# Kernel optimization log

Measured on AMD Instinct MI355X. Metric: run time of the kernel, lower is better.

The kernel has to match this reference:

```python
import jax, jax.numpy as jnp
import numpy as np

EMBED_DIM = 1024
NUM_HEADS = 16
HEAD_DIM = EMBED_DIM // NUM_HEADS


def setup_inputs() -> dict:
    key = jax.random.key(0)
    ks = jax.random.split(key, 9)
    B, S, E, hd = 2, 2048, EMBED_DIM, HEAD_DIM
    s_e = 1.0 / np.sqrt(E)
    return {
        "x": jax.random.normal(ks[0], (B, S, E), dtype=jnp.float32),
        "wq": jax.random.uniform(ks[1], (E, E), jnp.float32, -s_e, s_e),
        "bq": jax.random.uniform(ks[2], (E,), jnp.float32, -s_e, s_e),
        "wk": jax.random.uniform(ks[3], (E, hd), jnp.float32, -s_e, s_e),
        "bk": jax.random.uniform(ks[4], (hd,), jnp.float32, -s_e, s_e),
        "wv": jax.random.uniform(ks[5], (E, hd), jnp.float32, -s_e, s_e),
        "bv": jax.random.uniform(ks[6], (hd,), jnp.float32, -s_e, s_e),
        "wo": jax.random.uniform(ks[7], (E, E), jnp.float32, -s_e, s_e),
        "bo": jax.random.uniform(ks[8], (E,), jnp.float32, -s_e, s_e),
    }


def reference(x, wq, bq, wk, bk, wv, bv, wo, bo):
    B, S, E = x.shape
    H, hd = NUM_HEADS, HEAD_DIM
    # projections
    q = (x @ wq + bq).reshape(B, S, H, hd)          # [B,S,H,hd]
    k = x @ wk + bk                                  # [B,S,hd] shared across heads
    v = x @ wv + bv                                  # [B,S,hd]
    scale = 1.0 / np.sqrt(hd).astype(np.float32)
    # scores: [B,H,S_q,S_k]
    scores = jnp.einsum('bqhd,bkd->bhqk', q, k) * scale
    attn = jax.nn.softmax(scores, axis=-1)
    out = jnp.einsum('bhqk,bkd->bqhd', attn, v).reshape(B, S, E)
    return out @ wo + bo
```

## Files before the change

### kernel.cpp

```cpp
#include <hip/hip_runtime.h>
#include <stdint.h>

#define SLEN 2048
#define EDIM 1024
#define NH 16
#define HD 64
#define QLD 1152

typedef unsigned short u16;
typedef short bf8 __attribute__((ext_vector_type(8)));
typedef float f4 __attribute__((ext_vector_type(4)));
typedef bf8 bf8_a __attribute__((may_alias));
typedef uint2 uint2_a __attribute__((may_alias));
typedef uint4 uint4_a __attribute__((may_alias));

__device__ __forceinline__ u16 f2bf(float x) {
  union { __bf16 h; u16 u; } c; c.h = (__bf16)x; return c.u;
}
__device__ __forceinline__ unsigned pk2bf(float a, float b) {
  union { __bf16 h[2]; unsigned u; } c;
  c.h[0] = (__bf16)a; c.h[1] = (__bf16)b;
  return c.u;
}
__device__ __forceinline__ void async_cp16(u16* lds, const u16* g) {
  __builtin_amdgcn_global_load_lds((__attribute__((address_space(1))) void*)g,
                                   (__attribute__((address_space(3))) void*)lds,
                                   16, 0, 0);
}

__global__ void convert_x(const float* __restrict__ src, u16* __restrict__ dst) {
  const int i = (blockIdx.x * 256 + threadIdx.x) * 8;
  u16 tmp[8];
#pragma unroll
  for (int j = 0; j < 8; ++j) tmp[j] = f2bf(src[i + j]);
  *(uint4_a*)&dst[i] = *(const uint4_a*)tmp;
}

__device__ __forceinline__ void tcvt_tile(const float* src, int srcLd,
                                          u16* dst, int dstLd, int r0, int c0) {
  __shared__ u16 tile[64][65];
  const int t = threadIdx.x;
#pragma unroll
  for (int i = 0; i < 16; ++i) {
    int e = i * 256 + t, rr = e >> 6, cc = e & 63;
    tile[rr][cc] = f2bf(src[(size_t)(r0 + rr) * srcLd + c0 + cc]);
  }
  __syncthreads();
#pragma unroll
  for (int i = 0; i < 16; ++i) {
    int e = i * 256 + t, j = e >> 6, ii = e & 63;
    dst[(size_t)(c0 + j) * dstLd + r0 + ii] = tile[ii][j];
  }
}

__global__ void prep_w(const float* wq, const float* wk, const float* wv,
                       const float* wo, const float* bq, const float* bk,
                       const float* bv, const float* bo,
                       u16* wT, u16* woT, float* bQKV, float* bOut) {
  const int yy = blockIdx.y;
  if (yy < 16) tcvt_tile(wq, 1024, wT, 1024, blockIdx.x * 64, yy * 64);
  else if (yy < 32) tcvt_tile(wo, 1024, woT, 1024, blockIdx.x * 64, (yy - 16) * 64);
  else if (yy == 32) tcvt_tile(wk, 64, wT + (size_t)1024 * 1024, 1024, blockIdx.x * 64, 0);
  else if (yy == 33) tcvt_tile(wv, 64, wT + (size_t)1088 * 1024, 1024, blockIdx.x * 64, 0);
  else {
    int i = blockIdx.x * 256 + threadIdx.x;
    if (i < 1024) bQKV[i] = bq[i];
    else if (i < 1088) bQKV[i] = bk[i - 1024];
    else if (i < 1152) bQKV[i] = bv[i - 1088];
    int j = i - 1152;
    if (j >= 0 && j < 1024) bOut[j] = bo[j];
  }
}

__global__ __launch_bounds__(256) void gemm_bt_bias(
    const u16* __restrict__ A, const u16* __restrict__ Bt,
    const float* __restrict__ bias, void* __restrict__ C, int K, int ldc,
    int ofp32, u16* __restrict__ vtb) {
  __shared__ __align__(16) u16 As[64 * 64];
  __shared__ __align__(16) u16 Bs[128 * 64];
  const int tn0 = blockIdx.x * 128, tm0 = blockIdx.y * 64;
  const int tid = threadIdx.x, wave = tid >> 6, lane = tid & 63;
  const int quad = lane >> 4, l16 = lane & 15;
  const int wm = wave & 1, wn = wave >> 1;

  f4 acc[2][4];
#pragma unroll
  for (int i = 0; i < 2; ++i)
#pragma unroll
    for (int j = 0; j < 4; ++j) acc[i][j] = f4{0.f, 0.f, 0.f, 0.f};

  int aslot[2], bslot[4]; size_t aoff[2], boff[4];
#pragma unroll
  for (int i = 0; i < 2; ++i) {
    int s = i * 256 + tid, m = s >> 3, kc = s & 7, c = (kc - m) & 7;
    aslot[i] = s; aoff[i] = (size_t)(tm0 + m) * K + c * 8;
  }
#pragma unroll
  for (int i = 0; i < 4; ++i) {
    int s = i * 256 + tid, n = s >> 3, kc = s & 7, c = (kc - n) & 7;
    bslot[i] = s; boff[i] = (size_t)(tn0 + n) * K + c * 8;
  }
  int ard[2][2], brd[4][2];
#pragma unroll
  for (int mi = 0; mi < 2; ++mi) {
    int m = wm * 32 + mi * 16 + l16;
#pragma unroll
    for (int kk = 0; kk < 2; ++kk)
      ard[mi][kk] = (m * 8 + (((kk * 4 + quad) + m) & 7)) * 8;
  }
#pragma unroll
  for (int ni = 0; ni < 4; ++ni) {
    int n = wn * 64 + ni * 16 + l16;
#pragma unroll
    for (int kk = 0; kk < 2; ++kk)
      brd[ni][kk] = (n * 8 + (((kk * 4 + quad) + n) & 7)) * 8;
  }

  const int kIt = K >> 6;
  for (int it = 0; it < kIt; ++it) {
    __syncthreads();
    const size_t kb = (size_t)it * 64;
#pragma unroll
    for (int i = 0; i < 2; ++i) async_cp16(&As[aslot[i] * 8], A + aoff[i] + kb);
#pragma unroll
    for (int i = 0; i < 4; ++i) async_cp16(&Bs[bslot[i] * 8], Bt + boff[i] + kb);
    __syncthreads();
#pragma unroll
    for (int kk = 0; kk < 2; ++kk) {
      bf8 af[2], bfr[4];
#pragma unroll
      for (int mi = 0; mi < 2; ++mi) af[mi] = *(const bf8_a*)&As[ard[mi][kk]];
#pragma unroll
      for (int ni = 0; ni < 4; ++ni) bfr[ni] = *(const bf8_a*)&Bs[brd[ni][kk]];
#pragma unroll
      for (int mi = 0; mi < 2; ++mi)
#pragma unroll
        for (int ni = 0; ni < 4; ++ni)
          acc[mi][ni] = __builtin_amdgcn_mfma_f32_16x16x32_bf16(
              af[mi], bfr[ni], acc[mi][ni], 0, 0, 0);
    }
  }

  float bv[4];
#pragma unroll
  for (int ni = 0; ni < 4; ++ni) bv[ni] = bias[tn0 + wn * 64 + ni * 16 + l16];
#pragma unroll
  for (int mi = 0; mi < 2; ++mi) {
    int row0 = tm0 + wm * 32 + mi * 16 + quad * 4;
#pragma unroll
    for (int ni = 0; ni < 4; ++ni) {
      int col = tn0 + wn * 64 + ni * 16 + l16;
      float vv[4];
#pragma unroll
      for (int r = 0; r < 4; ++r) vv[r] = acc[mi][ni][r] + bv[ni];
      if (ofp32) {
#pragma unroll
        for (int r = 0; r < 4; ++r)
          ((float*)C)[(size_t)(row0 + r) * ldc + col] = vv[r];
      } else {
#pragma unroll
        for (int r = 0; r < 4; ++r)
          ((u16*)C)[(size_t)(row0 + r) * ldc + col] = f2bf(vv[r]);
      }
      if (vtb != nullptr && col >= 1088) {
        int d = col - 1088, bb = row0 >> 11, s0 = row0 & 2047;
        uint2 pk;
        pk.x = pk2bf(vv[0], vv[1]);
        pk.y = pk2bf(vv[2], vv[3]);
        *(uint2_a*)&vtb[(size_t)(bb * 64 + d) * SLEN + s0] = pk;
      }
    }
  }
}

__global__ __launch_bounds__(256, 4) void attn_kernel(
    const u16* __restrict__ qkv, const u16* __restrict__ vT,
    u16* __restrict__ aout) {
  __shared__ __align__(16) u16 Kf[8192];
  __shared__ __align__(16) u16 Vf[8192];
  __shared__ __align__(16) u16 Ps[4096];
  const int qt = blockIdx.x, bh = blockIdx.y, b = bh >> 4, h = bh & 15;
  const int tid = threadIdx.x, wave = tid >> 6, lane = tid & 63;
  const int quad = lane >> 4, l16 = lane & 15;

#pragma unroll
  for (int i = 0; i < 4; ++i) {
    int d = i * 256 + tid;
    int kk = d >> 9, g = (d >> 6) & 7, qd = (d >> 4) & 3, r16 = d & 15;
    async_cp16(&Kf[d * 8],
               qkv + (size_t)(b * SLEN + qt * 128 + g * 16 + r16) * QLD +
                   h * HD + (kk * 4 + qd) * 8);
  }
  __syncthreads();
  bf8 bq[2][2];
#pragma unroll
  for (int nt = 0; nt < 2; ++nt)
#pragma unroll
    for (int kk = 0; kk < 2; ++kk)
      bq[nt][kk] = *(const bf8_a*)&Kf[((kk * 8 + wave * 2 + nt) * 64 + lane) * 8];

  f4 acc_o[2][4];
#pragma unroll
  for (int i = 0; i < 2; ++i)
#pragma unroll
    for (int j = 0; j < 4; ++j) acc_o[i][j] = f4{0.f, 0.f, 0.f, 0.f};
  f4 lr4[2] = {f4{0.f, 0.f, 0.f, 0.f}, f4{0.f, 0.f, 0.f, 0.f}};
  const float C1 = 0.125f * 1.44269504089f;
  const int psb = wave * 1024;

  for (int kt = 0; kt < 16; ++kt) {
    __syncthreads();
#pragma unroll
    for (int i = 0; i < 4; ++i) {
      int d = i * 256 + tid;
      int kk = d >> 9, k8 = (d >> 6) & 7, qd = (d >> 4) & 3, r16 = d & 15;
      async_cp16(&Kf[d * 8],
                 qkv + (size_t)(b * SLEN + kt * 128 + k8 * 16 + r16) * QLD +
                     EDIM + (kk * 4 + qd) * 8);
    }
#pragma unroll
    for (int i = 0; i < 4; ++i) {
      int d = i * 256 + tid;
      int k4 = d >> 8, ni = (d >> 6) & 3, qd = (d >> 4) & 3, r16 = d & 15;
      async_cp16(&Vf[d * 8],
                 vT + (size_t)(b * 64 + ni * 16 + r16) * SLEN + kt * 128 +
                     (k4 * 4 + qd) * 8);
    }
    __syncthreads();

#pragma unroll
    for (int k4 = 0; k4 < 4; ++k4) {
      f4 st[2][2];
#pragma unroll
      for (int j = 0; j < 2; ++j)
#pragma unroll
        for (int nt = 0; nt < 2; ++nt) st[j][nt] = f4{0.f, 0.f, 0.f, 0.f};
#pragma unroll
      for (int kk = 0; kk < 2; ++kk)
#pragma unroll
        for (int j = 0; j < 2; ++j) {
          bf8 ak = *(const bf8_a*)&Kf[((kk * 8 + k4 * 2 + j) * 64 + lane) * 8];
#pragma unroll
          for (int nt = 0; nt < 2; ++nt)
            st[j][nt] = __builtin_amdgcn_mfma_f32_16x16x32_bf16(
                ak, bq[nt][kk], st[j][nt], 0, 0, 0);
        }
#pragma unroll
      for (int nt = 0; nt < 2; ++nt)
#pragma unroll
        for (int j = 0; j < 2; ++j) {
          f4 pe;
          pe[0] = __builtin_amdgcn_exp2f(st[j][nt][0] * C1);
          pe[1] = __builtin_amdgcn_exp2f(st[j][nt][1] * C1);
          pe[2] = __builtin_amdgcn_exp2f(st[j][nt][2] * C1);
          pe[3] = __builtin_amdgcn_exp2f(st[j][nt][3] * C1);
          lr4[nt] += pe;
          uint2 pk;
          pk.x = pk2bf(pe[0], pe[1]);
          pk.y = pk2bf(pe[2], pe[3]);
          int qd2 = j * 2 + (quad >> 1);
          *(uint2_a*)&Ps[psb + ((nt * 4 + qd2) * 16 + l16) * 8 + (quad & 1) * 4] = pk;
        }
      asm volatile("" ::: "memory");
      bf8 ap[2];
#pragma unroll
      for (int mt = 0; mt < 2; ++mt)
        ap[mt] = *(const bf8_a*)&Ps[psb + ((mt * 4 + quad) * 16 + l16) * 8];
#pragma unroll
      for (int ni = 0; ni < 4; ++ni) {
        bf8 bv = *(const bf8_a*)&Vf[((k4 * 4 + ni) * 64 + lane) * 8];
#pragma unroll
        for (int mt = 0; mt < 2; ++mt)
          acc_o[mt][ni] = __builtin_amdgcn_mfma_f32_16x16x32_bf16(
              ap[mt], bv, acc_o[mt][ni], 0, 0, 0);
      }
      asm volatile("" ::: "memory");
    }
  }

  float ls[2];
#pragma unroll
  for (int nt = 0; nt < 2; ++nt) {
    float s = (lr4[nt][0] + lr4[nt][1]) + (lr4[nt][2] + lr4[nt][3]);
    s += __shfl_xor(s, 16, 64);
    s += __shfl_xor(s, 32, 64);
    ls[nt] = s;
  }
#pragma unroll
  for (int mt = 0; mt < 2; ++mt)
#pragma unroll
    for (int r = 0; r < 4; ++r) {
      float li = __shfl(ls[mt], quad * 4 + r, 64);
      float inv = 1.f / li;
      size_t row = (size_t)(b * SLEN + qt * 128 + wave * 32 + mt * 16 + quad * 4 + r);
#pragma unroll
      for (int ni = 0; ni < 4; ++ni)
        aout[row * EDIM + h * HD + ni * 16 + l16] = f2bf(acc_o[mt][ni][r] * inv);
    }
}

extern "C" void kernel_launch(void* const* d_in, const int* in_sizes, int n_in,
                              void* d_out, int out_size, void* d_ws, size_t ws_size,
                              hipStream_t stream) {
  const float* x  = (const float*)d_in[0];
  const float* wq = (const float*)d_in[1];
  const float* bq = (const float*)d_in[2];
  const float* wk = (const float*)d_in[3];
  const float* bk = (const float*)d_in[4];
  const float* wv = (const float*)d_in[5];
  const float* bv = (const float*)d_in[6];
  const float* wo = (const float*)d_in[7];
  const float* bo = (const float*)d_in[8];

  char* ws = (char*)d_ws;
  size_t off = 0;
  auto carve = [&](size_t bytes) {
    void* p = ws + off;
    off = (off + bytes + 255) & ~(size_t)255;
    return p;
  };
  u16* xbf     = (u16*)carve((size_t)4096 * EDIM * 2);
  u16* wT      = (u16*)carve((size_t)1152 * 1024 * 2);
  u16* woT     = (u16*)carve((size_t)1024 * 1024 * 2);
  float* bQKV  = (float*)carve(1152 * 4);
  float* bOut  = (float*)carve(1024 * 4);
  u16* qkvb    = (u16*)carve((size_t)4096 * QLD * 2);
  u16* vTb     = (u16*)carve((size_t)2 * 64 * SLEN * 2);
  u16* aob     = (u16*)carve((size_t)4096 * EDIM * 2);

  convert_x<<<dim3(2048), 256, 0, stream>>>(x, xbf);
  prep_w<<<dim3(16, 35), 256, 0, stream>>>(wq, wk, wv, wo, bq, bk, bv, bo,
                                           wT, woT, bQKV, bOut);

  gemm_bt_bias<<<dim3(9, 64), 256, 0, stream>>>(xbf, wT, bQKV, qkvb, 1024, QLD,
                                                0, vTb);

  attn_kernel<<<dim3(16, 32), 256, 0, stream>>>(qkvb, vTb, aob);

  gemm_bt_bias<<<dim3(8, 64), 256, 0, stream>>>(aob, woT, bOut, d_out, 1024,
                                                1024, 1, nullptr);
}
```

Baseline: 183.7 us.

## Split attention over two key halves with a reduction kernel; fold x conversion into prep

The attention kernel now gets a third grid dimension that splits the 16 key tiles into two halves. Each half writes unnormalised bf16 partial outputs and per-row sums to a workspace, and a new reduce_o kernel adds the two halves and divides by the combined sum. This doubles the block count so more of the GPU is busy on the attention stage, at the cost of extra global traffic, one more launch and bf16 rounding of the partial results. The standalone x-to-bf16 conversion is also merged into the prep_w launch as extra grid rows, removing one kernel launch.

```diff
diff --git a/kernel.cpp b/kernel.cpp
--- a/kernel.cpp
+++ b/kernel.cpp
@@ -14,6 +14,9 @@
 typedef uint2 uint2_a __attribute__((may_alias));
 typedef uint4 uint4_a __attribute__((may_alias));
 
+__device__ __forceinline__ float bf2f(u16 u) {
+  union { unsigned u; float f; } c; c.u = ((unsigned)u) << 16; return c.f;
+}
 __device__ __forceinline__ u16 f2bf(float x) {
   union { __bf16 h; u16 u; } c; c.h = (__bf16)x; return c.u;
 }
@@ -28,14 +31,6 @@
                                    16, 0, 0);
 }
 
-__global__ void convert_x(const float* __restrict__ src, u16* __restrict__ dst) {
-  const int i = (blockIdx.x * 256 + threadIdx.x) * 8;
-  u16 tmp[8];
-#pragma unroll
-  for (int j = 0; j < 8; ++j) tmp[j] = f2bf(src[i + j]);
-  *(uint4_a*)&dst[i] = *(const uint4_a*)tmp;
-}
-
 __device__ __forceinline__ void tcvt_tile(const float* src, int srcLd,
                                           u16* dst, int dstLd, int r0, int c0) {
   __shared__ u16 tile[64][65];
@@ -55,20 +50,30 @@
 
 __global__ void prep_w(const float* wq, const float* wk, const float* wv,
                        const float* wo, const float* bq, const float* bk,
-                       const float* bv, const float* bo,
-                       u16* wT, u16* woT, float* bQKV, float* bOut) {
+                       const float* bv, const float* bo, const float* x,
+                       u16* wT, u16* woT, float* bQKV, float* bOut, u16* xbf) {
   const int yy = blockIdx.y;
   if (yy < 16) tcvt_tile(wq, 1024, wT, 1024, blockIdx.x * 64, yy * 64);
   else if (yy < 32) tcvt_tile(wo, 1024, woT, 1024, blockIdx.x * 64, (yy - 16) * 64);
   else if (yy == 32) tcvt_tile(wk, 64, wT + (size_t)1024 * 1024, 1024, blockIdx.x * 64, 0);
   else if (yy == 33) tcvt_tile(wv, 64, wT + (size_t)1088 * 1024, 1024, blockIdx.x * 64, 0);
-  else {
+  else if (yy == 34) {
     int i = blockIdx.x * 256 + threadIdx.x;
     if (i < 1024) bQKV[i] = bq[i];
     else if (i < 1088) bQKV[i] = bk[i - 1024];
     else if (i < 1152) bQKV[i] = bv[i - 1088];
     int j = i - 1152;
     if (j >= 0 && j < 1024) bOut[j] = bo[j];
+  } else {
+    const int blk = (yy - 35) * 16 + blockIdx.x, t = threadIdx.x;
+#pragma unroll
+    for (int i = 0; i < 8; ++i) {
+      int idx = blk * 16384 + i * 2048 + t * 8;
+      u16 tmp[8];
+#pragma unroll
+      for (int j = 0; j < 8; ++j) tmp[j] = f2bf(x[idx + j]);
+      *(uint4_a*)&xbf[idx] = *(const uint4_a*)tmp;
+    }
   }
 }
 
@@ -175,11 +180,12 @@
 
 __global__ __launch_bounds__(256, 4) void attn_kernel(
     const u16* __restrict__ qkv, const u16* __restrict__ vT,
-    u16* __restrict__ aout) {
+    u16* __restrict__ Opart, float* __restrict__ lpart) {
   __shared__ __align__(16) u16 Kf[8192];
   __shared__ __align__(16) u16 Vf[8192];
   __shared__ __align__(16) u16 Ps[4096];
-  const int qt = blockIdx.x, bh = blockIdx.y, b = bh >> 4, h = bh & 15;
+  const int qt = blockIdx.x, bh = blockIdx.y, ks = blockIdx.z;
+  const int b = bh >> 4, h = bh & 15;
   const int tid = threadIdx.x, wave = tid >> 6, lane = tid & 63;
   const int quad = lane >> 4, l16 = lane & 15;
 
@@ -208,7 +214,7 @@
   const float C1 = 0.125f * 1.44269504089f;
   const int psb = wave * 1024;
 
-  for (int kt = 0; kt < 16; ++kt) {
+  for (int kt = ks * 8; kt < ks * 8 + 8; ++kt) {
     __syncthreads();
 #pragma unroll
     for (int i = 0; i < 4; ++i) {
@@ -278,6 +284,7 @@
     }
   }
 
+  const size_t pbase = (size_t)((ks * 32 + bh) * 16 + qt) * 128;
   float ls[2];
 #pragma unroll
   for (int nt = 0; nt < 2; ++nt) {
@@ -285,18 +292,42 @@
     s += __shfl_xor(s, 16, 64);
     s += __shfl_xor(s, 32, 64);
     ls[nt] = s;
+    if (quad == 0) lpart[pbase + wave * 32 + nt * 16 + l16] = s;
   }
 #pragma unroll
   for (int mt = 0; mt < 2; ++mt)
 #pragma unroll
     for (int r = 0; r < 4; ++r) {
-      float li = __shfl(ls[mt], quad * 4 + r, 64);
-      float inv = 1.f / li;
-      size_t row = (size_t)(b * SLEN + qt * 128 + wave * 32 + mt * 16 + quad * 4 + r);
+      size_t row = pbase + wave * 32 + mt * 16 + quad * 4 + r;
 #pragma unroll
       for (int ni = 0; ni < 4; ++ni)
-        aout[row * EDIM + h * HD + ni * 16 + l16] = f2bf(acc_o[mt][ni][r] * inv);
-    }
+        Opart[row * 64 + ni * 16 + l16] = f2bf(acc_o[mt][ni][r]);
+    }
+}
+
+__global__ __launch_bounds__(256) void reduce_o(const u16* __restrict__ Op,
+                                                const float* __restrict__ lp,
+                                                u16* __restrict__ aob) {
+  const int qt = blockIdx.x, bh = blockIdx.y, b = bh >> 4, h = bh & 15;
+  const int t = threadIdx.x, r = t >> 1, dh = (t & 1) * 32;
+  const size_t p0 = (size_t)(bh * 16 + qt) * 128;
+  const size_t p1 = (size_t)((32 + bh) * 16 + qt) * 128;
+  const float inv = 1.f / (lp[p0 + r] + lp[p1 + r]);
+  const u16* o0 = Op + (p0 + r) * 64 + dh;
+  const u16* o1 = Op + (p1 + r) * 64 + dh;
+  u16* dst = aob + (size_t)(b * SLEN + qt * 128 + r) * EDIM + h * HD + dh;
+#pragma unroll
+  for (int c = 0; c < 4; ++c) {
+    uint4 a = *(const uint4_a*)(o0 + c * 8);
+    uint4 bb = *(const uint4_a*)(o1 + c * 8);
+    const u16* pa = (const u16*)&a;
+    const u16* pb = (const u16*)&bb;
+    u16 outv[8];
+#pragma unroll
+    for (int j = 0; j < 8; ++j)
+      outv[j] = f2bf((bf2f(pa[j]) + bf2f(pb[j])) * inv);
+    *(uint4_a*)(dst + c * 8) = *(const uint4_a*)outv;
+  }
 }
 
 extern "C" void kernel_launch(void* const* d_in, const int* in_sizes, int n_in,
@@ -327,15 +358,17 @@
   u16* qkvb    = (u16*)carve((size_t)4096 * QLD * 2);
   u16* vTb     = (u16*)carve((size_t)2 * 64 * SLEN * 2);
   u16* aob     = (u16*)carve((size_t)4096 * EDIM * 2);
-
-  convert_x<<<dim3(2048), 256, 0, stream>>>(x, xbf);
-  prep_w<<<dim3(16, 35), 256, 0, stream>>>(wq, wk, wv, wo, bq, bk, bv, bo,
-                                           wT, woT, bQKV, bOut);
+  u16* Opart   = (u16*)carve((size_t)2 * 32 * 16 * 128 * 64 * 2);
+  float* lpart = (float*)carve((size_t)2 * 32 * 16 * 128 * 4);
+
+  prep_w<<<dim3(16, 51), 256, 0, stream>>>(wq, wk, wv, wo, bq, bk, bv, bo, x,
+                                           wT, woT, bQKV, bOut, xbf);
 
   gemm_bt_bias<<<dim3(9, 64), 256, 0, stream>>>(xbf, wT, bQKV, qkvb, 1024, QLD,
                                                 0, vTb);
 
-  attn_kernel<<<dim3(16, 32), 256, 0, stream>>>(qkvb, vTb, aob);
+  attn_kernel<<<dim3(16, 32, 2), 256, 0, stream>>>(qkvb, vTb, Opart, lpart);
+  reduce_o<<<dim3(16, 32), 256, 0, stream>>>(Opart, lpart, aob);
 
   gemm_bt_bias<<<dim3(8, 64), 256, 0, stream>>>(aob, woT, bOut, d_out, 1024,
                                                 1024, 1, nullptr);
```

New measurement: 181.9 us. No clear change (-1.0%).

## Split attention over keys and fuse x conversion and partial merge into GEMMs

Applied to the files above, without the earlier changes.

Removes the separate fp32->bf16 conversion kernel for x by converting on the fly in the QKV GEMM's A-tile load. Attention now uses 64-row query tiles, 128-thread blocks and a two-way split over the key dimension, writing unnormalized partial outputs and row sums. The output-projection GEMM merges the two partials and normalizes while staging its A tile. This adds parallelism and removes a launch, at the cost of extra partial-output traffic and synchronous register-staged loads in place of async copies.

```diff
diff --git a/kernel.cpp b/kernel.cpp
--- a/kernel.cpp
+++ b/kernel.cpp
@@ -13,7 +13,11 @@
 typedef bf8 bf8_a __attribute__((may_alias));
 typedef uint2 uint2_a __attribute__((may_alias));
 typedef uint4 uint4_a __attribute__((may_alias));
-
+typedef float4 float4_a __attribute__((may_alias));
+
+__device__ __forceinline__ float bf2f(u16 u) {
+  union { unsigned u; float f; } c; c.u = ((unsigned)u) << 16; return c.f;
+}
 __device__ __forceinline__ u16 f2bf(float x) {
   union { __bf16 h; u16 u; } c; c.h = (__bf16)x; return c.u;
 }
@@ -26,14 +30,6 @@
   __builtin_amdgcn_global_load_lds((__attribute__((address_space(1))) void*)g,
                                    (__attribute__((address_space(3))) void*)lds,
                                    16, 0, 0);
-}
-
-__global__ void convert_x(const float* __restrict__ src, u16* __restrict__ dst) {
-  const int i = (blockIdx.x * 256 + threadIdx.x) * 8;
-  u16 tmp[8];
-#pragma unroll
-  for (int j = 0; j < 8; ++j) tmp[j] = f2bf(src[i + j]);
-  *(uint4_a*)&dst[i] = *(const uint4_a*)tmp;
 }
 
 __device__ __forceinline__ void tcvt_tile(const float* src, int srcLd,
@@ -72,12 +68,13 @@
   }
 }
 
-__global__ __launch_bounds__(256) void gemm_bt_bias(
-    const u16* __restrict__ A, const u16* __restrict__ Bt,
-    const float* __restrict__ bias, void* __restrict__ C, int K, int ldc,
-    int ofp32, u16* __restrict__ vtb) {
+__global__ __launch_bounds__(256) void gemm_qkv(
+    const float* __restrict__ X, const u16* __restrict__ Bt,
+    const float* __restrict__ bias, u16* __restrict__ C,
+    u16* __restrict__ vtb) {
   __shared__ __align__(16) u16 As[64 * 64];
   __shared__ __align__(16) u16 Bs[128 * 64];
+  const int K = 1024;
   const int tn0 = blockIdx.x * 128, tm0 = blockIdx.y * 64;
   const int tid = threadIdx.x, wave = tid >> 6, lane = tid & 63;
   const int quad = lane >> 4, l16 = lane & 15;
@@ -116,12 +113,21 @@
       brd[ni][kk] = (n * 8 + (((kk * 4 + quad) + n) & 7)) * 8;
   }
 
-  const int kIt = K >> 6;
-  for (int it = 0; it < kIt; ++it) {
-    __syncthreads();
+  for (int it = 0; it < 16; ++it) {
     const size_t kb = (size_t)it * 64;
-#pragma unroll
-    for (int i = 0; i < 2; ++i) async_cp16(&As[aslot[i] * 8], A + aoff[i] + kb);
+    uint4 staged[2];
+#pragma unroll
+    for (int i = 0; i < 2; ++i) {
+      float4 f0 = *(const float4_a*)(X + aoff[i] + kb);
+      float4 f1 = *(const float4_a*)(X + aoff[i] + kb + 4);
+      staged[i].x = pk2bf(f0.x, f0.y);
+      staged[i].y = pk2bf(f0.z, f0.w);
+      staged[i].z = pk2bf(f1.x, f1.y);
+      staged[i].w = pk2bf(f1.z, f1.w);
+    }
+    __syncthreads();
+#pragma unroll
+    for (int i = 0; i < 2; ++i) *(uint4_a*)&As[aslot[i] * 8] = staged[i];
 #pragma unroll
     for (int i = 0; i < 4; ++i) async_cp16(&Bs[bslot[i] * 8], Bt + boff[i] + kb);
     __syncthreads();
@@ -153,16 +159,10 @@
       float vv[4];
 #pragma unroll
       for (int r = 0; r < 4; ++r) vv[r] = acc[mi][ni][r] + bv[ni];
-      if (ofp32) {
-#pragma unroll
-        for (int r = 0; r < 4; ++r)
-          ((float*)C)[(size_t)(row0 + r) * ldc + col] = vv[r];
-      } else {
-#pragma unroll
-        for (int r = 0; r < 4; ++r)
-          ((u16*)C)[(size_t)(row0 + r) * ldc + col] = f2bf(vv[r]);
-      }
-      if (vtb != nullptr && col >= 1088) {
+#pragma unroll
+      for (int r = 0; r < 4; ++r)
+        C[(size_t)(row0 + r) * QLD + col] = f2bf(vv[r]);
+      if (col >= 1088) {
         int d = col - 1088, bb = row0 >> 11, s0 = row0 & 2047;
         uint2 pk;
         pk.x = pk2bf(vv[0], vv[1]);
@@ -173,31 +173,32 @@
   }
 }
 
-__global__ __launch_bounds__(256, 4) void attn_kernel(
+__global__ __launch_bounds__(128, 6) void attn_kernel(
     const u16* __restrict__ qkv, const u16* __restrict__ vT,
-    u16* __restrict__ aout) {
-  __shared__ __align__(16) u16 Kf[8192];
-  __shared__ __align__(16) u16 Vf[8192];
-  __shared__ __align__(16) u16 Ps[4096];
-  const int qt = blockIdx.x, bh = blockIdx.y, b = bh >> 4, h = bh & 15;
+    u16* __restrict__ Opart, float* __restrict__ lpart) {
+  __shared__ __align__(16) u16 Kf[4096];
+  __shared__ __align__(16) u16 Vf[4096];
+  __shared__ __align__(16) u16 Ps[2048];
+  const int qt = blockIdx.x, bh = blockIdx.y, ks = blockIdx.z;
+  const int b = bh >> 4, h = bh & 15;
   const int tid = threadIdx.x, wave = tid >> 6, lane = tid & 63;
   const int quad = lane >> 4, l16 = lane & 15;
 
 #pragma unroll
   for (int i = 0; i < 4; ++i) {
-    int d = i * 256 + tid;
-    int kk = d >> 9, g = (d >> 6) & 7, qd = (d >> 4) & 3, r16 = d & 15;
-    async_cp16(&Kf[d * 8],
-               qkv + (size_t)(b * SLEN + qt * 128 + g * 16 + r16) * QLD +
-                   h * HD + (kk * 4 + qd) * 8);
+    int d = i * 128 + tid;
+    int kk = d >> 8, g = (d >> 6) & 3, qd = (d >> 4) & 3, r16 = d & 15;
+    u16* dst = (kk == 0) ? &Kf[d * 8] : &Vf[(d - 256) * 8];
+    async_cp16(dst, qkv + (size_t)(b * SLEN + qt * 64 + g * 16 + r16) * QLD +
+                        h * HD + (kk * 4 + qd) * 8);
   }
   __syncthreads();
   bf8 bq[2][2];
 #pragma unroll
-  for (int nt = 0; nt < 2; ++nt)
-#pragma unroll
-    for (int kk = 0; kk < 2; ++kk)
-      bq[nt][kk] = *(const bf8_a*)&Kf[((kk * 8 + wave * 2 + nt) * 64 + lane) * 8];
+  for (int nt = 0; nt < 2; ++nt) {
+    bq[nt][0] = *(const bf8_a*)&Kf[((wave * 2 + nt) * 64 + lane) * 8];
+    bq[nt][1] = *(const bf8_a*)&Vf[((wave * 2 + nt) * 64 + lane) * 8];
+  }
 
   f4 acc_o[2][4];
 #pragma unroll
@@ -208,28 +209,28 @@
   const float C1 = 0.125f * 1.44269504089f;
   const int psb = wave * 1024;
 
-  for (int kt = 0; kt < 16; ++kt) {
+  for (int kt = ks * 16; kt < ks * 16 + 16; ++kt) {
     __syncthreads();
 #pragma unroll
     for (int i = 0; i < 4; ++i) {
-      int d = i * 256 + tid;
-      int kk = d >> 9, k8 = (d >> 6) & 7, qd = (d >> 4) & 3, r16 = d & 15;
+      int d = i * 128 + tid;
+      int kk = d >> 8, kg = (d >> 6) & 3, qd = (d >> 4) & 3, r16 = d & 15;
       async_cp16(&Kf[d * 8],
-                 qkv + (size_t)(b * SLEN + kt * 128 + k8 * 16 + r16) * QLD +
+                 qkv + (size_t)(b * SLEN + kt * 64 + kg * 16 + r16) * QLD +
                      EDIM + (kk * 4 + qd) * 8);
     }
 #pragma unroll
     for (int i = 0; i < 4; ++i) {
-      int d = i * 256 + tid;
+      int d = i * 128 + tid;
       int k4 = d >> 8, ni = (d >> 6) & 3, qd = (d >> 4) & 3, r16 = d & 15;
       async_cp16(&Vf[d * 8],
-                 vT + (size_t)(b * 64 + ni * 16 + r16) * SLEN + kt * 128 +
+                 vT + (size_t)(b * 64 + ni * 16 + r16) * SLEN + kt * 64 +
                      (k4 * 4 + qd) * 8);
     }
     __syncthreads();
 
 #pragma unroll
-    for (int k4 = 0; k4 < 4; ++k4) {
+    for (int k4 = 0; k4 < 2; ++k4) {
       f4 st[2][2];
 #pragma unroll
       for (int j = 0; j < 2; ++j)
@@ -239,7 +240,7 @@
       for (int kk = 0; kk < 2; ++kk)
 #pragma unroll
         for (int j = 0; j < 2; ++j) {
-          bf8 ak = *(const bf8_a*)&Kf[((kk * 8 + k4 * 2 + j) * 64 + lane) * 8];
+          bf8 ak = *(const bf8_a*)&Kf[((kk * 4 + k4 * 2 + j) * 64 + lane) * 8];
 #pragma unroll
           for (int nt = 0; nt < 2; ++nt)
             st[j][nt] = __builtin_amdgcn_mfma_f32_16x16x32_bf16(
@@ -278,6 +279,7 @@
     }
   }
 
+  const size_t pbase = (size_t)(ks * 32 + bh) * 2048 + qt * 64;
   float ls[2];
 #pragma unroll
   for (int nt = 0; nt < 2; ++nt) {
@@ -285,18 +287,122 @@
     s += __shfl_xor(s, 16, 64);
     s += __shfl_xor(s, 32, 64);
     ls[nt] = s;
+    if (quad == 0) lpart[pbase + wave * 32 + nt * 16 + l16] = s;
   }
 #pragma unroll
   for (int mt = 0; mt < 2; ++mt)
 #pragma unroll
     for (int r = 0; r < 4; ++r) {
-      float li = __shfl(ls[mt], quad * 4 + r, 64);
-      float inv = 1.f / li;
-      size_t row = (size_t)(b * SLEN + qt * 128 + wave * 32 + mt * 16 + quad * 4 + r);
+      size_t row = pbase + wave * 32 + mt * 16 + quad * 4 + r;
 #pragma unroll
       for (int ni = 0; ni < 4; ++ni)
-        aout[row * EDIM + h * HD + ni * 16 + l16] = f2bf(acc_o[mt][ni][r] * inv);
-    }
+        Opart[row * 64 + ni * 16 + l16] = f2bf(acc_o[mt][ni][r]);
+    }
+}
+
+__global__ __launch_bounds__(256) void gemm_out(
+    const u16* __restrict__ Op, const float* __restrict__ lp,
+    const u16* __restrict__ Bt, const float* __restrict__ bias,
+    float* __restrict__ C) {
+  __shared__ __align__(16) u16 As[64 * 64];
+  __shared__ __align__(16) u16 Bs[128 * 64];
+  const int K = 1024;
+  const int tn0 = blockIdx.x * 128, tm0 = blockIdx.y * 64;
+  const int tid = threadIdx.x, wave = tid >> 6, lane = tid & 63;
+  const int quad = lane >> 4, l16 = lane & 15;
+  const int wm = wave & 1, wn = wave >> 1;
+
+  f4 acc[2][4];
+#pragma unroll
+  for (int i = 0; i < 2; ++i)
+#pragma unroll
+    for (int j = 0; j < 4; ++j) acc[i][j] = f4{0.f, 0.f, 0.f, 0.f};
+
+  int aslot[2]; size_t obase[2]; int lbase[2];
+#pragma unroll
+  for (int i = 0; i < 2; ++i) {
+    int s = i * 256 + tid, m = s >> 3, kc = s & 7, c = (kc - m) & 7;
+    aslot[i] = s;
+    int rowg = tm0 + m, b = rowg >> 11, qrow = rowg & 2047;
+    obase[i] = (size_t)b * 2097152 + (size_t)qrow * 64 + c * 8;
+    lbase[i] = b * 32768 + qrow;
+  }
+  int bslot[4]; size_t boff[4];
+#pragma unroll
+  for (int i = 0; i < 4; ++i) {
+    int s = i * 256 + tid, n = s >> 3, kc = s & 7, c = (kc - n) & 7;
+    bslot[i] = s; boff[i] = (size_t)(tn0 + n) * K + c * 8;
+  }
+  int ard[2][2], brd[4][2];
+#pragma unroll
+  for (int mi = 0; mi < 2; ++mi) {
+    int m = wm * 32 + mi * 16 + l16;
+#pragma unroll
+    for (int kk = 0; kk < 2; ++kk)
+      ard[mi][kk] = (m * 8 + (((kk * 4 + quad) + m) & 7)) * 8;
+  }
+#pragma unroll
+  for (int ni = 0; ni < 4; ++ni) {
+    int n = wn * 64 + ni * 16 + l16;
+#pragma unroll
+    for (int kk = 0; kk < 2; ++kk)
+      brd[ni][kk] = (n * 8 + (((kk * 4 + quad) + n) & 7)) * 8;
+  }
+
+  for (int it = 0; it < 16; ++it) {
+    uint4 staged[2];
+#pragma unroll
+    for (int i = 0; i < 2; ++i) {
+      uint4 a0 = *(const uint4_a*)(Op + obase[i] + (size_t)it * 131072);
+      uint4 a1 = *(const uint4_a*)(Op + obase[i] + (size_t)it * 131072 + 4194304);
+      float l0 = lp[lbase[i] + it * 2048];
+      float l1 = lp[lbase[i] + 65536 + it * 2048];
+      float inv = 1.f / (l0 + l1);
+      const u16* pa = (const u16*)&a0;
+      const u16* pb = (const u16*)&a1;
+      u16 tmp[8];
+#pragma unroll
+      for (int j = 0; j < 8; ++j)
+        tmp[j] = f2bf((bf2f(pa[j]) + bf2f(pb[j])) * inv);
+      staged[i] = *(const uint4_a*)tmp;
+    }
+    __syncthreads();
+#pragma unroll
+    for (int i = 0; i < 2; ++i) *(uint4_a*)&As[aslot[i] * 8] = staged[i];
+#pragma unroll
+    for (int i = 0; i < 4; ++i)
+      async_cp16(&Bs[bslot[i] * 8], Bt + boff[i] + (size_t)it * 64);
+    __syncthreads();
+#pragma unroll
+    for (int kk = 0; kk < 2; ++kk) {
+      bf8 af[2], bfr[4];
+#pragma unroll
+      for (int mi = 0; mi < 2; ++mi) af[mi] = *(const bf8_a*)&As[ard[mi][kk]];
+#pragma unroll
+      for (int ni = 0; ni < 4; ++ni) bfr[ni] = *(const bf8_a*)&Bs[brd[ni][kk]];
+#pragma unroll
+      for (int mi = 0; mi < 2; ++mi)
+#pragma unroll
+        for (int ni = 0; ni < 4; ++ni)
+          acc[mi][ni] = __builtin_amdgcn_mfma_f32_16x16x32_bf16(
+              af[mi], bfr[ni], acc[mi][ni], 0, 0, 0);
+    }
+  }
+
+  float bv[4];
+#pragma unroll
+  for (int ni = 0; ni < 4; ++ni) bv[ni] = bias[tn0 + wn * 64 + ni * 16 + l16];
+#pragma unroll
+  for (int mi = 0; mi < 2; ++mi) {
+    int row0 = tm0 + wm * 32 + mi * 16 + quad * 4;
+#pragma unroll
+    for (int ni = 0; ni < 4; ++ni) {
+      int col = tn0 + wn * 64 + ni * 16 + l16;
+#pragma unroll
+      for (int r = 0; r < 4; ++r)
+        C[(size_t)(row0 + r) * 1024 + col] = acc[mi][ni][r] + bv[ni];
+    }
+  }
 }
 
 extern "C" void kernel_launch(void* const* d_in, const int* in_sizes, int n_in,
@@ -319,24 +425,22 @@
     off = (off + bytes + 255) & ~(size_t)255;
     return p;
   };
-  u16* xbf     = (u16*)carve((size_t)4096 * EDIM * 2);
   u16* wT      = (u16*)carve((size_t)1152 * 1024 * 2);
   u16* woT     = (u16*)carve((size_t)1024 * 1024 * 2);
   float* bQKV  = (float*)carve(1152 * 4);
   float* bOut  = (float*)carve(1024 * 4);
   u16* qkvb    = (u16*)carve((size_t)4096 * QLD * 2);
   u16* vTb     = (u16*)carve((size_t)2 * 64 * SLEN * 2);
-  u16* aob     = (u16*)carve((size_t)4096 * EDIM * 2);
-
-  convert_x<<<dim3(2048), 256, 0, stream>>>(x, xbf);
+  u16* Opart   = (u16*)carve((size_t)2 * 32 * 2048 * 64 * 2);
+  float* lpart = (float*)carve((size_t)2 * 32 * 2048 * 4);
+
   prep_w<<<dim3(16, 35), 256, 0, stream>>>(wq, wk, wv, wo, bq, bk, bv, bo,
                                            wT, woT, bQKV, bOut);
 
-  gemm_bt_bias<<<dim3(9, 64), 256, 0, stream>>>(xbf, wT, bQKV, qkvb, 1024, QLD,
-                                                0, vTb);
-
-  attn_kernel<<<dim3(16, 32), 256, 0, stream>>>(qkvb, vTb, aob);
-
-  gemm_bt_bias<<<dim3(8, 64), 256, 0, stream>>>(aob, woT, bOut, d_out, 1024,
-                                                1024, 1, nullptr);
-}
+  gemm_qkv<<<dim3(9, 64), 256, 0, stream>>>(x, wT, bQKV, qkvb, vTb);
+
+  attn_kernel<<<dim3(32, 32, 2), 128, 0, stream>>>(qkvb, vTb, Opart, lpart);
+
+  gemm_out<<<dim3(8, 64), 256, 0, stream>>>(Opart, lpart, woT, bOut,
+                                            (float*)d_out);
+}
```

Result: slower. 216.9 us (+18.1%).
